# Kernel tuning notes

Measured on AMD Instinct MI355X. Metric: run time of the kernel, lower is better.

Reference implementation:

```python
import jax, jax.numpy as jnp
import numpy as np

B, C, H, W = 4, 64, 160, 160
OUT = 64
KS = (5, 7)


def conv2d(x, w, b=None, pad=0, groups=1):
    y = jax.lax.conv_general_dilated(
        x, w, (1, 1), [(pad, pad), (pad, pad)],
        feature_group_count=groups,
        dimension_numbers=('NCHW', 'OIHW', 'NCHW'))
    return y if b is None else y + b[None, :, None, None]


def bn_eval(x, g, b, m, v, eps=1e-5):
    s = g / jnp.sqrt(v + eps)
    return x * s[None, :, None, None] + (b - m * s)[None, :, None, None]


def boundary_attn(x, w1, b1, w2, b2):
    Cc = x.shape[1]
    kx = jnp.array([[-1., 0., 1.], [-2., 0., 2.], [-1., 0., 1.]], jnp.float32)
    ky = jnp.array([[-1., -2., -1.], [0., 0., 0.], [1., 2., 1.]], jnp.float32)
    sobel = jnp.concatenate([jnp.tile(kx[None, None], (Cc, 1, 1, 1)),
                             jnp.tile(ky[None, None], (Cc, 1, 1, 1))], axis=0)  # [2C,1,3,3]
    # grouped conv (groups=C): same output-channel grouping semantics as torch
    edge = jnp.abs(conv2d(x, sobel, pad=1, groups=Cc))
    edge = (edge[:, :Cc] + edge[:, Cc:]).mean(axis=1, keepdims=True)
    a = jax.nn.relu(conv2d(x, w1, b1, pad=1))
    a = conv2d(a, w2, b2, pad=0)
    a = jax.nn.sigmoid(a + edge)
    return x * a + x


def icc(off, half_k):
    # iterative cumulative constraint over the (small, static) K channel axis
    K = off.shape[1]
    cs = [None] * K
    cs[half_k] = off[:, half_k]
    for i in range(1, half_k + 1):
        cs[half_k - i] = 0.5 * cs[half_k - i + 1] + 0.5 * off[:, half_k - i]
        cs[half_k + i] = 0.5 * cs[half_k + i - 1] + 0.5 * off[:, half_k + i]
    c = jnp.stack(cs, axis=1)
    w = jnp.ones((K, 1, 3, 3), jnp.float32) / 9.0
    return conv2d(c, w, pad=1, groups=K)


def tumor_center(x):
    _, _, Hx, Wx = x.shape
    fs = x.mean(axis=1)  # [B,H,W]
    hg = jnp.arange(Hx, dtype=x.dtype)[None, :, None]
    wg = jnp.arange(Wx, dtype=x.dtype)[None, None, :]
    tot = fs.sum(axis=(1, 2)) + 1e-6
    return (fs * hg).sum(axis=(1, 2)) / tot, (fs * wg).sum(axis=(1, 2)) / tot


def dyn1d(x, kw, kb, K, O):
    # Original Dynamic1DConv reshapes x to [B*H*W, C, 1, 1] and grid_samples a
    # [1,K] grid per pixel. With align_corners=True a 1x1 input maps every grid
    # coordinate to ix=iy=0, so sampled[n,c,k] == x[b,c,h,w] for all k; the
    # bmm with per-pixel kernels followed by sum over C therefore collapses to
    # (sum_c x) * (sum_k kernels) -- same math, no giant gather materialized.
    Bx, _, Hx, Wx = x.shape
    ker = conv2d(x, kw, kb, pad=0).reshape(Bx, O, K, Hx, Wx)
    return x.sum(axis=1, keepdims=True) * ker.sum(axis=2)


def reference(x, ba_w1, ba_b1, ba_w2, ba_b2,
              off_w1, off_b1, off_bn_g, off_bn_b, off_bn_m, off_bn_v,
              off_w2, off_b2,
              rk5_w, rk5_b, rk7_w, rk7_b,
              lk5_w, lk5_b, lk7_w, lk7_b,
              sf_w, sf_b, sf_bn_g, sf_bn_b, sf_bn_m, sf_bn_v,
              fc_w, fc_b):
    residual = x  # in_channels == out_channels -> nn.Identity
    xa = boundary_attn(x, ba_w1, ba_b1, ba_w2, ba_b2)
    # offset branch (faithful to original; mathematically dead because the
    # per-pixel grid_sample ignores its grid -- see dyn1d). BN in eval mode.
    raw = conv2d(xa, off_w1, off_b1, pad=1)
    raw = jax.nn.relu(bn_eval(raw, off_bn_g, off_bn_b, off_bn_m, off_bn_v))
    raw = conv2d(raw, off_w2, off_b2, pad=1)
    sumk, idx = sum(KS), 0
    _offs = []
    for k in KS:
        _offs.append(icc(jnp.tanh(raw[:, idx:idx + k]), k // 2))
        _offs.append(icc(jnp.tanh(raw[:, sumk + idx:sumk + idx + k]), k // 2))
        idx += k
    _hc, _wc = tumor_center(xa)  # also dead w.r.t. output
    O = OUT // 2 // len(KS)  # 16 channels per scale per flow type
    feats = [dyn1d(xa, rk5_w, rk5_b, 5, O), dyn1d(xa, rk7_w, rk7_b, 7, O),
             dyn1d(xa, lk5_w, lk5_b, 5, O), dyn1d(xa, lk7_w, lk7_b, 7, O)]
    fusion = jnp.concatenate(feats, axis=1)  # [B, OUT, H, W]
    y = jax.nn.relu(bn_eval(conv2d(fusion, sf_w, sf_b, pad=1),
                            sf_bn_g, sf_bn_b, sf_bn_m, sf_bn_v))
    y = conv2d(y, fc_w, fc_b, pad=0)
    return y + residual


def setup_inputs() -> dict:
    key = jax.random.key(0)
    keys = iter(jax.random.split(key, 40))
    def nrm(shape, s=0.05):
        return jax.random.normal(next(keys), shape, jnp.float32) * s
    d = {}
    d['x'] = nrm((B, C, H, W), 1.0)
    d['ba_w1'] = nrm((C // 2, C, 3, 3)); d['ba_b1'] = nrm((C // 2,))
    d['ba_w2'] = nrm((1, C // 2, 1, 1)); d['ba_b2'] = nrm((1,))
    d['off_w1'] = nrm((C // 2, C, 3, 3)); d['off_b1'] = nrm((C // 2,))
    d['off_bn_g'] = 1.0 + nrm((C // 2,)); d['off_bn_b'] = nrm((C // 2,))
    d['off_bn_m'] = nrm((C // 2,))
    d['off_bn_v'] = jax.random.uniform(next(keys), (C // 2,), jnp.float32, 0.5, 1.5)
    d['off_w2'] = nrm((2 * sum(KS), C // 2, 3, 3)); d['off_b2'] = nrm((2 * sum(KS),))
    O = OUT // 2 // len(KS)
    for name, k in (('rk5', 5), ('rk7', 7), ('lk5', 5), ('lk7', 7)):
        d[name + '_w'] = nrm((O * k, C, 1, 1)); d[name + '_b'] = nrm((O * k,))
    d['sf_w'] = nrm((OUT, OUT, 3, 3)); d['sf_b'] = nrm((OUT,))
    d['sf_bn_g'] = 1.0 + nrm((OUT,)); d['sf_bn_b'] = nrm((OUT,))
    d['sf_bn_m'] = nrm((OUT,))
    d['sf_bn_v'] = jax.random.uniform(next(keys), (OUT,), jnp.float32, 0.5, 1.5)
    d['fc_w'] = nrm((OUT, OUT, 1, 1)); d['fc_b'] = nrm((OUT,))
    return d
```

## Files before the change

### kernel.cpp

```cpp
#include <hip/hip_runtime.h>
#include <hip/hip_bf16.h>
#include <math.h>

#define BB 4
#define CC 64
#define HH 160
#define WW 160
#define HWs (HH*WW)
#define NPIX (BB*HWs)

using bf16 = __hip_bfloat16;
typedef __attribute__((ext_vector_type(8)))  short short8v;
typedef __attribute__((ext_vector_type(16))) float float16v;

__device__ __forceinline__ unsigned short f2bfu(float f){
    union { bf16 h; unsigned short u; } cv; cv.h = __float2bfloat16(f); return cv.u;
}
__device__ __forceinline__ float bfu2f(unsigned short u){
    union { float f; unsigned int i; } cv; cv.i = ((unsigned int)u)<<16; return cv.f;
}
__device__ __forceinline__ float16v fzero16(){
    float16v z;
    #pragma unroll
    for(int i=0;i<16;i++) z[i]=0.f;
    return z;
}

constexpr int B1X1 = 0;
constexpr int SFBo = 64;
constexpr int SFWf = 128;
constexpr int BAWf = 18560;
constexpr int FUWf = 27776;
constexpr int FCWf = 29824;
constexpr int WS_FLOATS = 31872;

__global__ void k_prep(const float* __restrict__ rk5w, const float* __restrict__ rk5b,
                       const float* __restrict__ rk7w, const float* __restrict__ rk7b,
                       const float* __restrict__ lk5w, const float* __restrict__ lk5b,
                       const float* __restrict__ lk7w, const float* __restrict__ lk7b,
                       const float* __restrict__ sfw,  const float* __restrict__ sfb,
                       const float* __restrict__ bng,  const float* __restrict__ bnb,
                       const float* __restrict__ bnm,  const float* __restrict__ bnv,
                       const float* __restrict__ baw1, const float* __restrict__ fcw,
                       float* __restrict__ ws)
{
    int tid = blockIdx.x*blockDim.x + threadIdx.x;
    int nt  = gridDim.x*blockDim.x;
    for(int o=tid;o<64;o+=nt){
        int grp=o>>4, oo=o&15; int K=(grp&1)?7:5;
        const float* bp = (grp==0)?rk5b:(grp==1)?rk7b:(grp==2)?lk5b:lk7b;
        float s=0.f; for(int k=0;k<K;k++) s += bp[oo*K+k];
        ws[B1X1+o]=s;
    }
    for(int oc=tid;oc<64;oc+=nt){
        float sc = bng[oc]*rsqrtf(bnv[oc]+1e-5f);
        ws[SFBo+oc] = sfb[oc]*sc + bnb[oc] - bnm[oc]*sc;
    }
    unsigned short* sfwf = (unsigned short*)(ws + SFWf);
    for(int idx=tid; idx<36864; idx+=nt){
        int og = idx/18432;  int rem = idx - og*18432;
        int f  = rem>>9;     int r2 = rem & 511;
        int lane = r2>>3;    int j = r2&7;
        int tap = f>>2, kc = f&3;
        int oc = og*32 + (lane&31);
        int ic = kc*16 + (lane>>5)*8 + j;
        float sc = bng[oc]*rsqrtf(bnv[oc]+1e-5f);
        sfwf[idx] = f2bfu(sfw[(oc*64+ic)*9 + tap] * sc);
    }
    unsigned short* bawf = (unsigned short*)(ws + BAWf);
    for(int idx=tid; idx<18432; idx+=nt){
        int f  = idx>>9;     int r2 = idx & 511;
        int lane = r2>>3;    int j = r2&7;
        int tap = f>>2, kc = f&3;
        int oc = lane&31;
        int ic = kc*16 + (lane>>5)*8 + j;
        bawf[idx] = f2bfu(baw1[(oc*64+ic)*9 + tap]);
    }
    unsigned short* fuwf = (unsigned short*)(ws + FUWf);
    for(int idx=tid; idx<4096; idx+=nt){
        int og   = idx>>11;
        int kc   = (idx>>9)&3;
        int lane = (idx>>3)&63;
        int j    = idx&7;
        int oc = og*32 + (lane&31);
        int c  = kc*16 + (lane>>5)*8 + j;
        int grp = oc>>4, oo = oc&15; int K = (grp&1)?7:5;
        const float* w = (grp==0)?rk5w:(grp==1)?rk7w:(grp==2)?lk5w:lk7w;
        float s = 0.f;
        for(int k=0;k<K;k++) s += w[(oo*K+k)*64 + c];
        fuwf[idx] = f2bfu(s);
    }
    unsigned short* fcwf = (unsigned short*)(ws + FCWf);
    for(int idx=tid; idx<4096; idx+=nt){
        int og   = idx>>11;
        int kc   = (idx>>9)&3;
        int lane = (idx>>3)&63;
        int j    = idx&7;
        int oc = og*32 + (lane&31);
        int c  = kc*16 + (lane>>5)*8 + j;
        fcwf[idx] = f2bfu(fcw[oc*64 + c]);
    }
}

__global__ __launch_bounds__(256)
void k_x2nhwc(const float* __restrict__ x, unsigned short* __restrict__ xb)
{
    __shared__ unsigned short ls[128*72];
    const int t = threadIdx.x;
    const int p0 = blockIdx.x*128;
    const int b = p0 / HWs, pp0 = p0 % HWs;
    const float4* xb4 = (const float4*)(x + (size_t)b*CC*HWs + pp0);
    #pragma unroll
    for(int iter=0; iter<8; iter++){
        int idx = iter*256 + t;
        int c = idx>>5, g = idx&31;
        float4 v = xb4[(size_t)c*(HWs/4) + g];
        int px = g*4;
        int bs = (c>>3) ^ ((g>>1)&7);
        unsigned short* base = ls + bs*8 + (c&7);
        base[(px+0)*72] = f2bfu(v.x);
        base[(px+1)*72] = f2bfu(v.y);
        base[(px+2)*72] = f2bfu(v.z);
        base[(px+3)*72] = f2bfu(v.w);
    }
    __syncthreads();
    #pragma unroll
    for(int iter=0; iter<4; iter++){
        int idx = iter*256 + t;
        int sub = idx&7, px = idx>>3;
        int bs = sub ^ ((px>>3)&7);
        short8v v = *(short8v*)(ls + px*72 + bs*8);
        *(short8v*)(xb + ((size_t)(p0+px))*64 + sub*8) = v;
    }
}

__global__ __launch_bounds__(256)
void k_fuseA(const unsigned short* __restrict__ xb, const float* __restrict__ bab1,
             const float* __restrict__ baw2, const float* __restrict__ bab2,
             const float* __restrict__ ws, unsigned short* __restrict__ fus)
{
    __shared__ unsigned short tile[10*18*72];
    __shared__ float ebuf[2][128];
    const int bw = blockIdx.x, bh = blockIdx.y, b = blockIdx.z;
    const int t = threadIdx.x;
    const int wave = t>>6, lane = t&63;
    const int half = lane>>5, n = lane&31;
    const int w0 = bw*16, h0 = bh*8;

    const unsigned short* fb = xb + (size_t)b*HWs*64;
    for(int idx=t; idx<1440; idx+=256){
        int sub = idx&7; int pix = idx>>3;
        int row = pix/18, col = pix%18;
        int gh = h0-1+row, gw = w0-1+col;
        short8v v = {0,0,0,0,0,0,0,0};
        if(gh>=0&&gh<HH&&gw>=0&&gw<WW)
            v = *(const short8v*)(fb + ((size_t)(gh*WW+gw))*64 + sub*8);
        *(short8v*)(tile + (row*18+col)*72 + sub*8) = v;
    }
    float b1v[16], w2v[16];
    #pragma unroll
    for(int r=0;r<16;r++){
        int oc = (r&3) + 8*(r>>2) + 4*half;
        b1v[r] = bab1[oc];
        w2v[r] = baw2[oc];
    }
    __syncthreads();

    const int row = 2*wave + (n>>4), col = n&15;

    float cz;
    {
        const unsigned short* bawf = (const unsigned short*)(ws + BAWf);
        float16v acc = fzero16();
        #pragma unroll
        for(int kc=0; kc<4; kc++){
            short8v af[9];
            #pragma unroll
            for(int tap=0; tap<9; tap++)
                af[tap] = *(const short8v*)(bawf + (((size_t)(tap*4+kc))*64 + lane)*8);
            #pragma unroll
            for(int tap=0; tap<9; tap++){
                const int dh = tap/3, dw = tap%3;
                short8v bf = *(const short8v*)(tile + ((row+dh)*18 + col+dw)*72
                                               + kc*16 + half*8);
                acc = __builtin_amdgcn_mfma_f32_32x32x16_bf16(af[tap], bf, acc, 0,0,0);
            }
        }
        cz = 0.f;
        #pragma unroll
        for(int r=0;r<16;r++) cz += fmaxf(acc[r]+b1v[r],0.f)*w2v[r];
        cz += __shfl_xor(cz, 32);
    }
    float sx;
    {
        short8v ones;
        #pragma unroll
        for(int j=0;j<8;j++) ones[j] = (short)0x3F80;
        float16v s = fzero16();
        #pragma unroll
        for(int kc=0; kc<4; kc++){
            short8v bf = *(const short8v*)(tile + ((row+1)*18 + col+1)*72 + kc*16 + half*8);
            s = __builtin_amdgcn_mfma_f32_32x32x16_bf16(ones, bf, s, 0,0,0);
        }
        sx = s[0];
    }
    {
        const int hf = t>>7, px = t&127;
        const int r = px>>4, c = px&15;
        float e = 0.f;
        #pragma unroll
        for(int s=0; s<4; s++){
            const int sub = hf*4 + s;
            if(hf==0){
                short8v a0 = *(const short8v*)(tile + ((r  )*18 + c  )*72 + sub*8);
                short8v a2 = *(const short8v*)(tile + ((r  )*18 + c+2)*72 + sub*8);
                short8v a3 = *(const short8v*)(tile + ((r+1)*18 + c  )*72 + sub*8);
                short8v a5 = *(const short8v*)(tile + ((r+1)*18 + c+2)*72 + sub*8);
                short8v a6 = *(const short8v*)(tile + ((r+2)*18 + c  )*72 + sub*8);
                short8v a8 = *(const short8v*)(tile + ((r+2)*18 + c+2)*72 + sub*8);
                #pragma unroll
                for(int j=0;j<8;j++){
                    float gx = (bfu2f((unsigned short)a2[j]) - bfu2f((unsigned short)a0[j]))
                       + 2.f*(bfu2f((unsigned short)a5[j]) - bfu2f((unsigned short)a3[j]))
                       +      (bfu2f((unsigned short)a8[j]) - bfu2f((unsigned short)a6[j]));
                    e += fabsf(gx);
                }
            } else {
                short8v b0 = *(const short8v*)(tile + ((r  )*18 + c  )*72 + sub*8);
                short8v b1 = *(const short8v*)(tile + ((r  )*18 + c+1)*72 + sub*8);
                short8v b2 = *(const short8v*)(tile + ((r  )*18 + c+2)*72 + sub*8);
                short8v b6 = *(const short8v*)(tile + ((r+2)*18 + c  )*72 + sub*8);
                short8v b7 = *(const short8v*)(tile + ((r+2)*18 + c+1)*72 + sub*8);
                short8v b8 = *(const short8v*)(tile + ((r+2)*18 + c+2)*72 + sub*8);
                #pragma unroll
                for(int j=0;j<8;j++){
                    float gy = (bfu2f((unsigned short)b6[j]) - bfu2f((unsigned short)b0[j]))
                       + 2.f*(bfu2f((unsigned short)b7[j]) - bfu2f((unsigned short)b1[j]))
                       +      (bfu2f((unsigned short)b8[j]) - bfu2f((unsigned short)b2[j]));
                    e += fabsf(gy);
                }
            }
        }
        ebuf[hf][px] = e;
    }
    __syncthreads();

    const int pxl = row*16 + col;
    float z = cz + bab2[0] + (ebuf[0][pxl] + ebuf[1][pxl]) * (1.f/32.f);
    float A = 1.f + 1.f/(1.f+__expf(-z));
    float Q = A * sx;
    float P = A * Q;

    const unsigned short* fuwf = (const unsigned short*)(ws + FUWf);
    #pragma unroll
    for(int og=0; og<2; og++){
        float16v a = fzero16();
        #pragma unroll
        for(int kc=0; kc<4; kc++){
            short8v wf = *(const short8v*)(fuwf + (((size_t)og*4 + kc)*64 + lane)*8);
            short8v bf = *(const short8v*)(tile + ((row+1)*18 + col+1)*72 + kc*16 + half*8);
            a = __builtin_amdgcn_mfma_f32_32x32x16_bf16(wf, bf, a, 0,0,0);
        }
        float bq[16];
        #pragma unroll
        for(int r=0;r<16;r++) bq[r] = ws[B1X1 + og*32 + (r&3)+8*(r>>2)+4*half];
        unsigned short* base = fus + ((size_t)b*HWs + (h0+row)*WW + w0+col)*64
                               + og*32 + 4*half;
        #pragma unroll
        for(int g=0; g<4; g++){
            union { unsigned long long u; unsigned short s[4]; } pk;
            #pragma unroll
            for(int rr=0; rr<4; rr++)
                pk.s[rr] = f2bfu(P*a[4*g+rr] + Q*bq[4*g+rr]);
            *(unsigned long long*)(base + 8*g) = pk.u;
        }
    }
}

__global__ __launch_bounds__(256)
void k_fuseB(const unsigned short* __restrict__ fus, const float* __restrict__ ws,
             const float* __restrict__ fcb, const float* __restrict__ x,
             float* __restrict__ out)
{
    __shared__ unsigned short ftile[10*18*72];
    const int bw = blockIdx.x, bh = blockIdx.y, b = blockIdx.z;
    const int t  = threadIdx.x;
    const int wave = t>>6, lane = t&63;
    const int half = lane>>5, n = lane&31;
    const int w0 = bw*16, h0 = bh*8;

    const unsigned short* fb = fus + (size_t)b*HWs*64;
    for(int idx=t; idx<1440; idx+=256){
        int sub = idx&7; int pix = idx>>3;
        int row = pix/18, col = pix%18;
        int gh = h0-1+row, gw = w0-1+col;
        short8v v = {0,0,0,0,0,0,0,0};
        if(gh>=0&&gh<HH&&gw>=0&&gw<WW)
            v = *(const short8v*)(fb + ((size_t)(gh*WW+gw))*64 + sub*8);
        *(short8v*)(ftile + (row*18+col)*72 + sub*8) = v;
    }
    __syncthreads();

    const int row = 2*wave + (n>>4), col = n&15;
    const unsigned short* sfwf = (const unsigned short*)(ws + SFWf);
    const unsigned short* fcwf = (const unsigned short*)(ws + FCWf);
    float16v F0 = fzero16(), F1 = fzero16();

    #pragma unroll
    for(int og=0; og<2; og++){
        float16v Y = fzero16();
        #pragma unroll
        for(int kc=0; kc<4; kc++){
            short8v af[9];
            #pragma unroll
            for(int tap=0; tap<9; tap++)
                af[tap] = *(const short8v*)(sfwf + (((size_t)og*36 + tap*4+kc)*64 + lane)*8);
            #pragma unroll
            for(int tap=0; tap<9; tap++){
                const int dh = tap/3, dw = tap%3;
                short8v bf = *(const short8v*)(ftile + ((row+dh)*18 + col+dw)*72
                                               + kc*16 + half*8);
                Y = __builtin_amdgcn_mfma_f32_32x32x16_bf16(af[tap], bf, Y, 0,0,0);
            }
        }
        unsigned short yb[16];
        #pragma unroll
        for(int r=0;r<16;r++){
            float bias = ws[SFBo + og*32 + (r&3)+8*(r>>2)+4*half];
            yb[r] = f2bfu(fmaxf(Y[r] + bias, 0.f));
        }
        #pragma unroll
        for(int kcl=0; kcl<2; kcl++){
            const int kc_fc = 2*og + kcl;
            unsigned short l0,l1,l2,l3, s0,s1,s2,s3;
            if(half==0){ l0=yb[8*kcl+0]; l1=yb[8*kcl+1]; l2=yb[8*kcl+2]; l3=yb[8*kcl+3];
                         s0=yb[8*kcl+4]; s1=yb[8*kcl+5]; s2=yb[8*kcl+6]; s3=yb[8*kcl+7]; }
            else       { l0=yb[8*kcl+4]; l1=yb[8*kcl+5]; l2=yb[8*kcl+6]; l3=yb[8*kcl+7];
                         s0=yb[8*kcl+0]; s1=yb[8*kcl+1]; s2=yb[8*kcl+2]; s3=yb[8*kcl+3]; }
            int p0 = (int)((unsigned)s0 | ((unsigned)s1<<16));
            int p1 = (int)((unsigned)s2 | ((unsigned)s3<<16));
            int r0 = __shfl_xor(p0, 32);
            int r1 = __shfl_xor(p1, 32);
            unsigned short m0 = (unsigned short)(r0 & 0xffff);
            unsigned short m1 = (unsigned short)(((unsigned)r0) >> 16);
            unsigned short m2 = (unsigned short)(r1 & 0xffff);
            unsigned short m3 = (unsigned short)(((unsigned)r1) >> 16);
            short8v B;
            if(half==0){ B[0]=(short)l0; B[1]=(short)l1; B[2]=(short)l2; B[3]=(short)l3;
                         B[4]=(short)m0; B[5]=(short)m1; B[6]=(short)m2; B[7]=(short)m3; }
            else       { B[0]=(short)m0; B[1]=(short)m1; B[2]=(short)m2; B[3]=(short)m3;
                         B[4]=(short)l0; B[5]=(short)l1; B[6]=(short)l2; B[7]=(short)l3; }
            short8v fa0 = *(const short8v*)(fcwf + (((size_t)0*4 + kc_fc)*64 + lane)*8);
            short8v fa1 = *(const short8v*)(fcwf + (((size_t)1*4 + kc_fc)*64 + lane)*8);
            F0 = __builtin_amdgcn_mfma_f32_32x32x16_bf16(fa0, B, F0, 0,0,0);
            F1 = __builtin_amdgcn_mfma_f32_32x32x16_bf16(fa1, B, F1, 0,0,0);
        }
    }
    #pragma unroll
    for(int og=0; og<2; og++){
        #pragma unroll
        for(int r=0;r<16;r++){
            int oc = og*32 + (r&3)+8*(r>>2)+4*half;
            size_t g = ((size_t)(b*CC + oc))*HWs + (h0+row)*WW + w0 + col;
            float v = (og==0) ? F0[r] : F1[r];
            out[g] = v + fcb[oc] + x[g];
        }
    }
}

extern "C" void kernel_launch(void* const* d_in, const int* in_sizes, int n_in,
                              void* d_out, int out_size, void* d_ws, size_t ws_size,
                              hipStream_t stream)
{
    const float* x     = (const float*)d_in[0];
    const float* ba_w1 = (const float*)d_in[1];
    const float* ba_b1 = (const float*)d_in[2];
    const float* ba_w2 = (const float*)d_in[3];
    const float* ba_b2 = (const float*)d_in[4];
    const float* rk5_w = (const float*)d_in[13];
    const float* rk5_b = (const float*)d_in[14];
    const float* rk7_w = (const float*)d_in[15];
    const float* rk7_b = (const float*)d_in[16];
    const float* lk5_w = (const float*)d_in[17];
    const float* lk5_b = (const float*)d_in[18];
    const float* lk7_w = (const float*)d_in[19];
    const float* lk7_b = (const float*)d_in[20];
    const float* sf_w  = (const float*)d_in[21];
    const float* sf_b  = (const float*)d_in[22];
    const float* bng   = (const float*)d_in[23];
    const float* bnb   = (const float*)d_in[24];
    const float* bnm   = (const float*)d_in[25];
    const float* bnv   = (const float*)d_in[26];
    const float* fc_w  = (const float*)d_in[27];
    const float* fc_b  = (const float*)d_in[28];

    float* wsf = (float*)d_ws;
    unsigned short* XB  = (unsigned short*)((char*)d_ws + (size_t)WS_FLOATS*4);
    unsigned short* FUS = XB + (size_t)NPIX*64;
    float* out = (float*)d_out;

    k_prep<<<64, 256, 0, stream>>>(rk5_w,rk5_b,rk7_w,rk7_b,lk5_w,lk5_b,lk7_w,lk7_b,
                                   sf_w,sf_b,bng,bnb,bnm,bnv, ba_w1, fc_w, wsf);
    k_x2nhwc<<<NPIX/128, 256, 0, stream>>>(x, XB);
    k_fuseA<<<dim3(10,20,4), 256, 0, stream>>>(XB, ba_b1, ba_w2, ba_b2, wsf, FUS);
    k_fuseB<<<dim3(10,20,4), 256, 0, stream>>>(FUS, wsf, fc_b, x, out);
}
```

Before: 176.8 us.

## Fuse NCHW-to-NHWC conversion into fuseA and interleave MFMA accumulator chains

Drops the separate x-to-NHWC bf16 kernel. k_fuseA now reads fp32 NCHW x directly into its shared tile, converting and transposing there, which saves a full intermediate write and read plus one launch. In k_fuseA the 1x1, channel-sum and 3x3 MFMAs now share one k-loop. In k_fuseB the two output-group 3x3 convolutions run as two independent accumulator chains. The aim is more MFMA-level parallelism, at the cost of higher register pressure and uncoalesced scalar stores to LDS during tile loading.

```diff
diff --git a/kernel.cpp b/kernel.cpp
--- a/kernel.cpp
+++ b/kernel.cpp
@@ -103,39 +103,7 @@
 }
 
 __global__ __launch_bounds__(256)
-void k_x2nhwc(const float* __restrict__ x, unsigned short* __restrict__ xb)
-{
-    __shared__ unsigned short ls[128*72];
-    const int t = threadIdx.x;
-    const int p0 = blockIdx.x*128;
-    const int b = p0 / HWs, pp0 = p0 % HWs;
-    const float4* xb4 = (const float4*)(x + (size_t)b*CC*HWs + pp0);
-    #pragma unroll
-    for(int iter=0; iter<8; iter++){
-        int idx = iter*256 + t;
-        int c = idx>>5, g = idx&31;
-        float4 v = xb4[(size_t)c*(HWs/4) + g];
-        int px = g*4;
-        int bs = (c>>3) ^ ((g>>1)&7);
-        unsigned short* base = ls + bs*8 + (c&7);
-        base[(px+0)*72] = f2bfu(v.x);
-        base[(px+1)*72] = f2bfu(v.y);
-        base[(px+2)*72] = f2bfu(v.z);
-        base[(px+3)*72] = f2bfu(v.w);
-    }
-    __syncthreads();
-    #pragma unroll
-    for(int iter=0; iter<4; iter++){
-        int idx = iter*256 + t;
-        int sub = idx&7, px = idx>>3;
-        int bs = sub ^ ((px>>3)&7);
-        short8v v = *(short8v*)(ls + px*72 + bs*8);
-        *(short8v*)(xb + ((size_t)(p0+px))*64 + sub*8) = v;
-    }
-}
-
-__global__ __launch_bounds__(256)
-void k_fuseA(const unsigned short* __restrict__ xb, const float* __restrict__ bab1,
+void k_fuseA(const float* __restrict__ x, const float* __restrict__ bab1,
              const float* __restrict__ baw2, const float* __restrict__ bab2,
              const float* __restrict__ ws, unsigned short* __restrict__ fus)
 {
@@ -147,15 +115,32 @@
     const int half = lane>>5, n = lane&31;
     const int w0 = bw*16, h0 = bh*8;
 
-    const unsigned short* fb = xb + (size_t)b*HWs*64;
-    for(int idx=t; idx<1440; idx+=256){
-        int sub = idx&7; int pix = idx>>3;
-        int row = pix/18, col = pix%18;
-        int gh = h0-1+row, gw = w0-1+col;
-        short8v v = {0,0,0,0,0,0,0,0};
-        if(gh>=0&&gh<HH&&gw>=0&&gw<WW)
-            v = *(const short8v*)(fb + ((size_t)(gh*WW+gw))*64 + sub*8);
-        *(short8v*)(tile + (row*18+col)*72 + sub*8) = v;
+    const float* xp = x + (size_t)b*CC*HWs;
+    #pragma unroll
+    for(int i=0;i<10;i++){
+        int idx = i*256 + t;
+        int q = idx & 3, pr = idx >> 2;
+        int ch = pr/10, row = pr - ch*10;
+        int gh = h0-1+row;
+        float4 v = {0.f,0.f,0.f,0.f};
+        if((unsigned)gh < HH)
+            v = *(const float4*)(xp + (size_t)ch*HWs + gh*WW + w0 + q*4);
+        unsigned short* dst = tile + (row*18 + q*4 + 1)*72 + ch;
+        dst[0]     = f2bfu(v.x);
+        dst[72]    = f2bfu(v.y);
+        dst[144]   = f2bfu(v.z);
+        dst[216]   = f2bfu(v.w);
+    }
+    #pragma unroll
+    for(int i=0;i<5;i++){
+        int idx = i*256 + t;
+        int e = idx & 1, pr = idx >> 1;
+        int ch = pr/10, row = pr - ch*10;
+        int gh = h0-1+row;
+        int gw = e ? (w0+16) : (w0-1);
+        float v = 0.f;
+        if((unsigned)gh < HH && (unsigned)gw < WW) v = xp[(size_t)ch*HWs + gh*WW + gw];
+        tile[(row*18 + (e?17:0))*72 + ch] = f2bfu(v);
     }
     float b1v[16], w2v[16];
     #pragma unroll
@@ -168,42 +153,38 @@
 
     const int row = 2*wave + (n>>4), col = n&15;
 
-    float cz;
-    {
-        const unsigned short* bawf = (const unsigned short*)(ws + BAWf);
-        float16v acc = fzero16();
-        #pragma unroll
-        for(int kc=0; kc<4; kc++){
-            short8v af[9];
-            #pragma unroll
-            for(int tap=0; tap<9; tap++)
-                af[tap] = *(const short8v*)(bawf + (((size_t)(tap*4+kc))*64 + lane)*8);
-            #pragma unroll
-            for(int tap=0; tap<9; tap++){
-                const int dh = tap/3, dw = tap%3;
-                short8v bf = *(const short8v*)(tile + ((row+dh)*18 + col+dw)*72
-                                               + kc*16 + half*8);
-                acc = __builtin_amdgcn_mfma_f32_32x32x16_bf16(af[tap], bf, acc, 0,0,0);
-            }
-        }
-        cz = 0.f;
-        #pragma unroll
-        for(int r=0;r<16;r++) cz += fmaxf(acc[r]+b1v[r],0.f)*w2v[r];
-        cz += __shfl_xor(cz, 32);
-    }
-    float sx;
-    {
-        short8v ones;
-        #pragma unroll
-        for(int j=0;j<8;j++) ones[j] = (short)0x3F80;
-        float16v s = fzero16();
-        #pragma unroll
-        for(int kc=0; kc<4; kc++){
-            short8v bf = *(const short8v*)(tile + ((row+1)*18 + col+1)*72 + kc*16 + half*8);
-            s = __builtin_amdgcn_mfma_f32_32x32x16_bf16(ones, bf, s, 0,0,0);
-        }
-        sx = s[0];
-    }
+    const unsigned short* bawf = (const unsigned short*)(ws + BAWf);
+    const unsigned short* fuwf = (const unsigned short*)(ws + FUWf);
+    short8v ones;
+    #pragma unroll
+    for(int j=0;j<8;j++) ones[j] = (short)0x3F80;
+    float16v accA = fzero16(), accS = fzero16(), accD0 = fzero16(), accD1 = fzero16();
+    #pragma unroll
+    for(int kc=0; kc<4; kc++){
+        short8v wf0 = *(const short8v*)(fuwf + (((size_t)0*4 + kc)*64 + lane)*8);
+        short8v wf1 = *(const short8v*)(fuwf + (((size_t)1*4 + kc)*64 + lane)*8);
+        short8v bfc = *(const short8v*)(tile + ((row+1)*18 + col+1)*72 + kc*16 + half*8);
+        accS  = __builtin_amdgcn_mfma_f32_32x32x16_bf16(ones, bfc, accS, 0,0,0);
+        accD0 = __builtin_amdgcn_mfma_f32_32x32x16_bf16(wf0,  bfc, accD0, 0,0,0);
+        accD1 = __builtin_amdgcn_mfma_f32_32x32x16_bf16(wf1,  bfc, accD1, 0,0,0);
+        short8v af[9];
+        #pragma unroll
+        for(int tap=0; tap<9; tap++)
+            af[tap] = *(const short8v*)(bawf + (((size_t)(tap*4+kc))*64 + lane)*8);
+        #pragma unroll
+        for(int tap=0; tap<9; tap++){
+            const int dh = tap/3, dw = tap%3;
+            short8v bf = *(const short8v*)(tile + ((row+dh)*18 + col+dw)*72
+                                           + kc*16 + half*8);
+            accA = __builtin_amdgcn_mfma_f32_32x32x16_bf16(af[tap], bf, accA, 0,0,0);
+        }
+    }
+    float cz = 0.f;
+    #pragma unroll
+    for(int r=0;r<16;r++) cz += fmaxf(accA[r]+b1v[r],0.f)*w2v[r];
+    cz += __shfl_xor(cz, 32);
+    float sx = accS[0];
+
     {
         const int hf = t>>7, px = t&127;
         const int r = px>>4, c = px&15;
@@ -251,16 +232,9 @@
     float Q = A * sx;
     float P = A * Q;
 
-    const unsigned short* fuwf = (const unsigned short*)(ws + FUWf);
     #pragma unroll
     for(int og=0; og<2; og++){
-        float16v a = fzero16();
-        #pragma unroll
-        for(int kc=0; kc<4; kc++){
-            short8v wf = *(const short8v*)(fuwf + (((size_t)og*4 + kc)*64 + lane)*8);
-            short8v bf = *(const short8v*)(tile + ((row+1)*18 + col+1)*72 + kc*16 + half*8);
-            a = __builtin_amdgcn_mfma_f32_32x32x16_bf16(wf, bf, a, 0,0,0);
-        }
+        const float16v& a = og ? accD1 : accD0;
         float bq[16];
         #pragma unroll
         for(int r=0;r<16;r++) bq[r] = ws[B1X1 + og*32 + (r&3)+8*(r>>2)+4*half];
@@ -304,31 +278,37 @@
     const int row = 2*wave + (n>>4), col = n&15;
     const unsigned short* sfwf = (const unsigned short*)(ws + SFWf);
     const unsigned short* fcwf = (const unsigned short*)(ws + FCWf);
+
+    float16v Y0 = fzero16(), Y1 = fzero16();
+    #pragma unroll
+    for(int kc=0; kc<4; kc++){
+        short8v af0[9], af1[9];
+        #pragma unroll
+        for(int tap=0; tap<9; tap++){
+            af0[tap] = *(const short8v*)(sfwf + (((size_t)(     tap*4+kc))*64 + lane)*8);
+            af1[tap] = *(const short8v*)(sfwf + (((size_t)(36 + tap*4+kc))*64 + lane)*8);
+        }
+        #pragma unroll
+        for(int tap=0; tap<9; tap++){
+            const int dh = tap/3, dw = tap%3;
+            short8v bf = *(const short8v*)(ftile + ((row+dh)*18 + col+dw)*72
+                                           + kc*16 + half*8);
+            Y0 = __builtin_amdgcn_mfma_f32_32x32x16_bf16(af0[tap], bf, Y0, 0,0,0);
+            Y1 = __builtin_amdgcn_mfma_f32_32x32x16_bf16(af1[tap], bf, Y1, 0,0,0);
+        }
+    }
+    unsigned short yb0[16], yb1[16];
+    #pragma unroll
+    for(int r=0;r<16;r++){
+        int rr = (r&3)+8*(r>>2)+4*half;
+        yb0[r] = f2bfu(fmaxf(Y0[r] + ws[SFBo +      rr], 0.f));
+        yb1[r] = f2bfu(fmaxf(Y1[r] + ws[SFBo + 32 + rr], 0.f));
+    }
+
     float16v F0 = fzero16(), F1 = fzero16();
-
     #pragma unroll
     for(int og=0; og<2; og++){
-        float16v Y = fzero16();
-        #pragma unroll
-        for(int kc=0; kc<4; kc++){
-            short8v af[9];
-            #pragma unroll
-            for(int tap=0; tap<9; tap++)
-                af[tap] = *(const short8v*)(sfwf + (((size_t)og*36 + tap*4+kc)*64 + lane)*8);
-            #pragma unroll
-            for(int tap=0; tap<9; tap++){
-                const int dh = tap/3, dw = tap%3;
-                short8v bf = *(const short8v*)(ftile + ((row+dh)*18 + col+dw)*72
-                                               + kc*16 + half*8);
-                Y = __builtin_amdgcn_mfma_f32_32x32x16_bf16(af[tap], bf, Y, 0,0,0);
-            }
-        }
-        unsigned short yb[16];
-        #pragma unroll
-        for(int r=0;r<16;r++){
-            float bias = ws[SFBo + og*32 + (r&3)+8*(r>>2)+4*half];
-            yb[r] = f2bfu(fmaxf(Y[r] + bias, 0.f));
-        }
+        const unsigned short* yb = og ? yb1 : yb0;
         #pragma unroll
         for(int kcl=0; kcl<2; kcl++){
             const int kc_fc = 2*og + kcl;
@@ -395,13 +375,11 @@
     const float* fc_b  = (const float*)d_in[28];
 
     float* wsf = (float*)d_ws;
-    unsigned short* XB  = (unsigned short*)((char*)d_ws + (size_t)WS_FLOATS*4);
-    unsigned short* FUS = XB + (size_t)NPIX*64;
+    unsigned short* FUS = (unsigned short*)((char*)d_ws + (size_t)WS_FLOATS*4);
     float* out = (float*)d_out;
 
     k_prep<<<64, 256, 0, stream>>>(rk5_w,rk5_b,rk7_w,rk7_b,lk5_w,lk5_b,lk7_w,lk7_b,
                                    sf_w,sf_b,bng,bnb,bnm,bnv, ba_w1, fc_w, wsf);
-    k_x2nhwc<<<NPIX/128, 256, 0, stream>>>(x, XB);
-    k_fuseA<<<dim3(10,20,4), 256, 0, stream>>>(XB, ba_b1, ba_w2, ba_b2, wsf, FUS);
+    k_fuseA<<<dim3(10,20,4), 256, 0, stream>>>(x, ba_b1, ba_w2, ba_b2, wsf, FUS);
     k_fuseB<<<dim3(10,20,4), 256, 0, stream>>>(FUS, wsf, fc_b, x, out);
 }
```

New measurement: 187.2 us. 5.9% more time.
